# Optimization experiments

Hardware: AMD Instinct MI355X
Metric: run time of the kernel (lower is better)

The kernel has to match this reference:

```python
import jax, jax.numpy as jnp
import numpy as np

D_MODEL = 1024
NUM_HEADS = 16
D_K = D_MODEL // NUM_HEADS


def setup_inputs() -> dict:
    key = jax.random.key(0)
    ks = jax.random.split(key, 11)
    B, S = 2, 2048
    scale = 1.0 / np.sqrt(D_MODEL)
    inp = {
        "Q_in": jax.random.normal(ks[0], (B, S, D_MODEL), jnp.float32),
        "K_in": jax.random.normal(ks[1], (B, S, D_MODEL), jnp.float32),
        "V_in": jax.random.normal(ks[2], (B, S, D_MODEL), jnp.float32),
        "Wq": jax.random.normal(ks[3], (D_MODEL, D_MODEL), jnp.float32) * scale,
        "bq": jnp.zeros((D_MODEL,), jnp.float32),
        "Wk": jax.random.normal(ks[4], (D_MODEL, D_MODEL), jnp.float32) * scale,
        "bk": jnp.zeros((D_MODEL,), jnp.float32),
        "Wv": jax.random.normal(ks[5], (D_MODEL, D_MODEL), jnp.float32) * scale,
        "bv": jnp.zeros((D_MODEL,), jnp.float32),
        "Wfc": jax.random.normal(ks[6], (D_MODEL, D_MODEL), jnp.float32) * scale,
        "bfc": jnp.zeros((D_MODEL,), jnp.float32),
    }
    return inp


def _split_heads(x, B):
    # [B, S, D] -> [B, H, S, d_k]
    return x.reshape(B, -1, NUM_HEADS, D_K).transpose(0, 2, 1, 3)


def reference(Q_in, K_in, V_in, Wq, bq, Wk, bk, Wv, bv, Wfc, bfc):
    B = Q_in.shape[0]
    q = _split_heads(Q_in @ Wq + bq, B)
    k = _split_heads(K_in @ Wk + bk, B)
    v = _split_heads(V_in @ Wv + bv, B)
    # scaled dot-product attention (mask=None)
    scores = jnp.einsum("bhqd,bhkd->bhqk", q, k) / jnp.sqrt(jnp.float32(D_K))
    attn = jax.nn.softmax(scores, axis=-1)
    ctx = jnp.einsum("bhqk,bhkd->bhqd", attn, v)
    out = ctx.transpose(0, 2, 1, 3).reshape(B, -1, D_MODEL)
    out = out @ Wfc + bfc
    return out, attn
```

## Files before the change

### kernel.cpp

```cpp
#include <hip/hip_runtime.h>

typedef unsigned short u16;
typedef _Float16 f16;
typedef __attribute__((ext_vector_type(8))) f16 f16x8;
typedef __attribute__((ext_vector_type(4))) float f32x4;
typedef __attribute__((ext_vector_type(4))) u16 u16x4;
typedef __attribute__((ext_vector_type(8))) u16 u16x8;

__device__ __forceinline__ u16 f2h(float x){
  f16 h = (f16)x;
  return __builtin_bit_cast(u16, h);
}
__device__ __forceinline__ float h2f(u16 v){
  return (float)__builtin_bit_cast(f16, v);
}

__device__ __forceinline__ void stage16(const void* g, void* l){
  __builtin_amdgcn_global_load_lds(
      (const __attribute__((address_space(1))) unsigned*)g,
      (__attribute__((address_space(3))) unsigned*)l, 16, 0, 0);
}

__global__ __launch_bounds__(256) void convert_x3(
    const float* __restrict__ in0, const float* __restrict__ in1, const float* __restrict__ in2,
    u16* __restrict__ o0, u16* __restrict__ o1, u16* __restrict__ o2){
  const int b = blockIdx.x >> 12;
  const int i = (blockIdx.x & 4095) * 256 + threadIdx.x;
  const float* in = (b == 0) ? in0 : (b == 1) ? in1 : in2;
  u16* out = (b == 0) ? o0 : (b == 1) ? o1 : o2;
  f32x4 v = ((const f32x4*)in)[i];
  u16x4 h;
  #pragma unroll
  for (int j = 0; j < 4; j++) h[j] = f2h(v[j]);
  ((u16x4*)out)[i] = h;
}

__global__ __launch_bounds__(256) void transpose_w4(
    const float* __restrict__ W0, const float* __restrict__ W1,
    const float* __restrict__ W2, const float* __restrict__ W3,
    u16* __restrict__ t0, u16* __restrict__ t1, u16* __restrict__ t2, u16* __restrict__ t3){
  __shared__ float tile[64][68];
  const int z = blockIdx.z;
  const float* W = (z == 0) ? W0 : (z == 1) ? W1 : (z == 2) ? W2 : W3;
  u16* wt = (z == 0) ? t0 : (z == 1) ? t1 : (z == 2) ? t2 : t3;
  const int tid = threadIdx.x;
  const int k0 = blockIdx.y * 64, n0 = blockIdx.x * 64;
  #pragma unroll
  for (int g = 0; g < 4; g++){
    int flat4 = g * 256 + tid;
    int row = flat4 >> 4, c4 = flat4 & 15;
    f32x4 v = *(const f32x4*)&W[(size_t)(k0 + row) * 1024 + n0 + c4 * 4];
    *(f32x4*)&tile[row][c4 * 4] = v;
  }
  __syncthreads();
  const int n = tid >> 2, kc = (tid & 3) * 16;
  u16x8 o0, o1;
  #pragma unroll
  for (int j = 0; j < 8; j++){
    o0[j] = f2h(tile[kc + j][n]);
    o1[j] = f2h(tile[kc + 8 + j][n]);
  }
  u16* dst = &wt[(size_t)(n0 + n) * 1024 + k0 + kc];
  *(u16x8*)dst = o0;
  *(u16x8*)(dst + 8) = o1;
}

template<int MODE>
__device__ __forceinline__ void gemm_body(
    const u16* __restrict__ A, const u16* __restrict__ B,
    const float* __restrict__ bias,
    float* __restrict__ outF, u16* __restrict__ outH,
    int N, int K, int bx, int by)
{
  __shared__ u16 sA[128 * 32];
  __shared__ u16 sB[128 * 32];
  const int tid = threadIdx.x;
  const int wid = tid >> 6, lane = tid & 63;
  const int lm = lane & 15, lg = lane >> 4;
  const int bm = by * 128, bn = bx * 128;
  const int wrow = (wid >> 1) * 64, wcol = (wid & 1) * 64;
  const int srow = tid >> 2;
  const int skc  = (tid & 3) * 8;

  f32x4 acc[4][4] = {};

  for (int kt = 0; kt < K; kt += 32){
    {
      char* dA = (char*)sA + wid * 1024;
      char* dB = (char*)sB + wid * 1024;
      stage16(A + (size_t)(bm +      srow) * K + kt + skc, dA);
      stage16(A + (size_t)(bm + 64 + srow) * K + kt + skc, dA + 4096);
      stage16(B + (size_t)(bn +      srow) * K + kt + skc, dB);
      stage16(B + (size_t)(bn + 64 + srow) * K + kt + skc, dB + 4096);
    }
    __syncthreads();
    f16x8 af[4], bf[4];
    #pragma unroll
    for (int mf = 0; mf < 4; mf++)
      af[mf] = *(const f16x8*)&sA[(wrow + mf * 16 + lm) * 32 + lg * 8];
    #pragma unroll
    for (int nf = 0; nf < 4; nf++)
      bf[nf] = *(const f16x8*)&sB[(wcol + nf * 16 + lm) * 32 + lg * 8];
    #pragma unroll
    for (int mf = 0; mf < 4; mf++)
      #pragma unroll
      for (int nf = 0; nf < 4; nf++)
        acc[mf][nf] = __builtin_amdgcn_mfma_f32_16x16x32_f16(af[mf], bf[nf], acc[mf][nf], 0, 0, 0);
    __syncthreads();
  }

  #pragma unroll
  for (int mf = 0; mf < 4; mf++)
    #pragma unroll
    for (int nf = 0; nf < 4; nf++){
      const int n  = bn + wcol + nf * 16 + lm;
      const int mb = bm + wrow + mf * 16 + lg * 4;
      #pragma unroll
      for (int r = 0; r < 4; r++){
        const int m = mb + r;
        float v = acc[mf][nf][r] + ((MODE == 2) ? bias[m] : bias[n]);
        if constexpr (MODE == 0){
          outF[(size_t)m * N + n] = v;
        } else if constexpr (MODE == 1){
          const size_t idx = (((size_t)((m >> 11) * 16 + (n >> 6))) * 2048 + (m & 2047)) * 64 + (n & 63);
          outH[idx] = f2h(v);
        } else {
          const size_t idx = (((size_t)((n >> 11) * 16 + (m >> 6))) * 64 + (m & 63)) * 2048 + (n & 2047);
          outH[idx] = f2h(v);
        }
      }
    }
}

__global__ __launch_bounds__(256, 2) void gemm_qk(
    const u16* __restrict__ xq, const u16* __restrict__ wqt, const float* __restrict__ bq, u16* __restrict__ qh,
    const u16* __restrict__ xk, const u16* __restrict__ wkt, const float* __restrict__ bk, u16* __restrict__ kh){
  const int z = blockIdx.z;
  gemm_body<1>(z ? xk : xq, z ? wkt : wqt, z ? bk : bq, nullptr, z ? kh : qh,
               1024, 1024, blockIdx.x, blockIdx.y);
}

__global__ __launch_bounds__(256, 2) void gemm_v(
    const u16* __restrict__ wvt, const u16* __restrict__ xv, const float* __restrict__ bv, u16* __restrict__ vt){
  gemm_body<2>(wvt, xv, bv, nullptr, vt, 4096, 1024, blockIdx.x, blockIdx.y);
}

__global__ __launch_bounds__(256, 2) void gemm_fc(
    const u16* __restrict__ ctx, const u16* __restrict__ wft, const float* __restrict__ bfc, float* __restrict__ outF){
  gemm_body<0>(ctx, wft, bfc, outF, nullptr, 1024, 1024, blockIdx.x, blockIdx.y);
}

__global__ __launch_bounds__(256, 2) void attn_fused(
    const u16* __restrict__ qh_, const u16* __restrict__ kh_,
    const u16* __restrict__ vt_,
    float* __restrict__ attn_out, u16* __restrict__ ctx)
{
  constexpr int S = 2048;
  __shared__ __align__(16) char smem[4 * 16 * 520 * 2];
  __shared__ float sred[4][16];
  __shared__ float linv[16];
  const int tid = threadIdx.x, wid = tid >> 6, lane = tid & 63;
  const int lm = lane & 15, lg = lane >> 4;
  u16 (*pb)[520] = (u16 (*)[520])(smem + wid * (16 * 520 * 2));
  const int wg = blockIdx.x;
  const int xcd = wg & 7, li = wg >> 3;
  const int bh = (xcd << 2) + (li >> 7);
  const int q0 = (li & 127) * 16;
  const size_t base = (size_t)bh * S * 64;
  const u16* Qh = qh_ + base;
  const u16* Kh = kh_ + base;
  const u16* Vt = vt_ + base;
  float* Aout = attn_out + (size_t)bh * S * S;
  const int kbase = wid * 512;

  f16x8 qb[2];
  #pragma unroll
  for (int ks = 0; ks < 2; ks++)
    qb[ks] = *(const f16x8*)(Qh + (size_t)(q0 + lm) * 64 + ks * 32 + lg * 8);

  const float SCL2 = 0.18033688011112042f;

  float part = 0.0f;
  f32x4 cacc[4] = {};
  for (int nt2 = 0; nt2 < 16; nt2++){
    const int col0 = kbase + nt2 * 32;
    f16x8 vb[4];
    #pragma unroll
    for (int nf = 0; nf < 4; nf++)
      vb[nf] = *(const f16x8*)(Vt + (size_t)(nf * 16 + lm) * S + col0 + lg * 8);

    const u16* kp0 = Kh + (size_t)(col0 + lm) * 64 + lg * 8;
    const u16* kp1 = kp0 + 16 * 64;
    f16x8 k00 = *(const f16x8*)(kp0);
    f16x8 k01 = *(const f16x8*)(kp0 + 32);
    f16x8 k10 = *(const f16x8*)(kp1);
    f16x8 k11 = *(const f16x8*)(kp1 + 32);
    f32x4 c0 = {}, c1 = {};
    c0 = __builtin_amdgcn_mfma_f32_16x16x32_f16(k00, qb[0], c0, 0, 0, 0);
    c0 = __builtin_amdgcn_mfma_f32_16x16x32_f16(k01, qb[1], c0, 0, 0, 0);
    c1 = __builtin_amdgcn_mfma_f32_16x16x32_f16(k10, qb[0], c1, 0, 0, 0);
    c1 = __builtin_amdgcn_mfma_f32_16x16x32_f16(k11, qb[1], c1, 0, 0, 0);

    #pragma unroll
    for (int half = 0; half < 2; half++){
      f32x4 c = half ? c1 : c0;
      u16x4 hp;
      #pragma unroll
      for (int r = 0; r < 4; r++){
        float e = __builtin_amdgcn_exp2f(c[r] * SCL2);
        part += e;
        hp[r] = f2h(e);
      }
      *(u16x4*)&pb[lm][nt2 * 32 + half * 16 + lg * 4] = hp;
    }
    f16x8 pa = *(const f16x8*)&pb[lm][nt2 * 32 + lg * 8];
    #pragma unroll
    for (int nf = 0; nf < 4; nf++)
      cacc[nf] = __builtin_amdgcn_mfma_f32_16x16x32_f16(pa, vb[nf], cacc[nf], 0, 0, 0);
  }

  part += __shfl_xor(part, 16);
  part += __shfl_xor(part, 32);
  if (lane < 16) sred[wid][lm] = part;
  __syncthreads();
  if (tid < 16) linv[tid] = 1.0f / (sred[0][tid] + sred[1][tid] + sred[2][tid] + sred[3][tid]);
  __syncthreads();

  #pragma unroll 4
  for (int r = 0; r < 16; r++){
    u16x8 hv = *(const u16x8*)&pb[r][lane * 8];
    const float iv = linv[r];
    f32x4 lo = { h2f(hv[0]) * iv, h2f(hv[1]) * iv, h2f(hv[2]) * iv, h2f(hv[3]) * iv };
    f32x4 hi = { h2f(hv[4]) * iv, h2f(hv[5]) * iv, h2f(hv[6]) * iv, h2f(hv[7]) * iv };
    float* dst = Aout + (size_t)(q0 + r) * S + kbase + lane * 8;
    *(f32x4*)dst = lo;
    *(f32x4*)(dst + 4) = hi;
  }

  const float myinv = linv[lg * 4 + 0];
  (void)myinv;
  float iv4[4];
  #pragma unroll
  for (int r = 0; r < 4; r++) iv4[r] = linv[lg * 4 + r];

  __syncthreads();
  float (*cred)[64][20] = (float (*)[64][20])smem;
  #pragma unroll
  for (int nf = 0; nf < 4; nf++){
    f32x4 sc;
    #pragma unroll
    for (int r = 0; r < 4; r++) sc[r] = cacc[nf][r] * iv4[r];
    *(f32x4*)&cred[wid][nf * 16 + lm][lg * 4] = sc;
  }
  __syncthreads();
  const int b = bh >> 4, h = bh & 15;
  const int rd = lane;
  const int rq = wid * 4;
  f32x4 s0 = *(const f32x4*)&cred[0][rd][rq];
  f32x4 s1 = *(const f32x4*)&cred[1][rd][rq];
  f32x4 s2 = *(const f32x4*)&cred[2][rd][rq];
  f32x4 s3 = *(const f32x4*)&cred[3][rd][rq];
  #pragma unroll
  for (int j = 0; j < 4; j++){
    float v = s0[j] + s1[j] + s2[j] + s3[j];
    ctx[(size_t)(b * 2048 + q0 + rq + j) * 1024 + h * 64 + rd] = f2h(v);
  }
}

extern "C" void kernel_launch(void* const* d_in, const int* in_sizes, int n_in,
                              void* d_out, int out_size, void* d_ws, size_t ws_size,
                              hipStream_t stream) {
  const float* Qi  = (const float*)d_in[0];
  const float* Ki  = (const float*)d_in[1];
  const float* Vi  = (const float*)d_in[2];
  const float* Wq  = (const float*)d_in[3];
  const float* bq  = (const float*)d_in[4];
  const float* Wk  = (const float*)d_in[5];
  const float* bk  = (const float*)d_in[6];
  const float* Wv  = (const float*)d_in[7];
  const float* bv  = (const float*)d_in[8];
  const float* Wfc = (const float*)d_in[9];
  const float* bfc = (const float*)d_in[10];

  char* w = (char*)d_ws;
  const size_t P  = 8388608;
  const size_t PW = 2097152;
  u16* xq  = (u16*)(w + 0*P);
  u16* xk  = (u16*)(w + 1*P);
  u16* xv  = (u16*)(w + 2*P);
  u16* qh  = (u16*)(w + 3*P);
  u16* kh  = (u16*)(w + 4*P);
  u16* vt  = (u16*)(w + 5*P);
  u16* ctx = (u16*)(w + 6*P);
  char* w2 = w + 7*P;
  u16* wqt = (u16*)(w2 + 0*PW);
  u16* wkt = (u16*)(w2 + 1*PW);
  u16* wvt = (u16*)(w2 + 2*PW);
  u16* wft = (u16*)(w2 + 3*PW);

  float* outp  = (float*)d_out;
  float* attnp = outp + 4194304;

  convert_x3<<<12288, 256, 0, stream>>>(Qi, Ki, Vi, xq, xk, xv);
  transpose_w4<<<dim3(16, 16, 4), 256, 0, stream>>>(Wq, Wk, Wv, Wfc, wqt, wkt, wvt, wft);

  gemm_qk<<<dim3(8, 32, 2), 256, 0, stream>>>(xq, wqt, bq, qh, xk, wkt, bk, kh);
  gemm_v<<<dim3(32, 8), 256, 0, stream>>>(wvt, xv, bv, vt);
  attn_fused<<<4096, 256, 0, stream>>>(qh, kh, vt, attnp, ctx);
  gemm_fc<<<dim3(8, 32), 256, 0, stream>>>(ctx, wft, bfc, outp);
}
```

Measured before the change: 424.6 us.

## Merge V projection into QK GEMM launch and persist attention blocks with prefetch

The Q, K and V projection GEMMs now run as one launch, with blockIdx.z selecting the operand set and the V GEMM using swapped grid indices. The attention kernel drops from 4096 to 512 workgroups, and each workgroup loops over 8 query tiles. K/V fragments are prefetched two steps ahead in a triple-buffered register ring, and the attention row write-back uses narrower, more coalesced stores. The aim is to remove one kernel launch, cut per-block setup, and hide global load latency behind MFMA work, at the cost of higher register pressure and less parallelism in the attention grid.

```diff
diff --git a/kernel.cpp b/kernel.cpp
--- a/kernel.cpp
+++ b/kernel.cpp
@@ -132,23 +132,26 @@
     }
 }
 
-__global__ __launch_bounds__(256, 2) void gemm_qk(
+__global__ __launch_bounds__(256, 2) void gemm_qkv(
     const u16* __restrict__ xq, const u16* __restrict__ wqt, const float* __restrict__ bq, u16* __restrict__ qh,
-    const u16* __restrict__ xk, const u16* __restrict__ wkt, const float* __restrict__ bk, u16* __restrict__ kh){
+    const u16* __restrict__ xk, const u16* __restrict__ wkt, const float* __restrict__ bk, u16* __restrict__ kh,
+    const u16* __restrict__ wvt, const u16* __restrict__ xv, const float* __restrict__ bv, u16* __restrict__ vt){
   const int z = blockIdx.z;
-  gemm_body<1>(z ? xk : xq, z ? wkt : wqt, z ? bk : bq, nullptr, z ? kh : qh,
-               1024, 1024, blockIdx.x, blockIdx.y);
-}
-
-__global__ __launch_bounds__(256, 2) void gemm_v(
-    const u16* __restrict__ wvt, const u16* __restrict__ xv, const float* __restrict__ bv, u16* __restrict__ vt){
-  gemm_body<2>(wvt, xv, bv, nullptr, vt, 4096, 1024, blockIdx.x, blockIdx.y);
+  if (z == 2){
+    gemm_body<2>(wvt, xv, bv, nullptr, vt, 4096, 1024, blockIdx.y, blockIdx.x);
+  } else if (z == 1){
+    gemm_body<1>(xk, wkt, bk, nullptr, kh, 1024, 1024, blockIdx.x, blockIdx.y);
+  } else {
+    gemm_body<1>(xq, wqt, bq, nullptr, qh, 1024, 1024, blockIdx.x, blockIdx.y);
+  }
 }
 
 __global__ __launch_bounds__(256, 2) void gemm_fc(
     const u16* __restrict__ ctx, const u16* __restrict__ wft, const float* __restrict__ bfc, float* __restrict__ outF){
   gemm_body<0>(ctx, wft, bfc, outF, nullptr, 1024, 1024, blockIdx.x, blockIdx.y);
 }
+
+#define MFMA16(A, B, C) __builtin_amdgcn_mfma_f32_16x16x32_f16((A), (B), (C), 0, 0, 0)
 
 __global__ __launch_bounds__(256, 2) void attn_fused(
     const u16* __restrict__ qh_, const u16* __restrict__ kh_,
@@ -156,114 +159,131 @@
     float* __restrict__ attn_out, u16* __restrict__ ctx)
 {
   constexpr int S = 2048;
-  __shared__ __align__(16) char smem[4 * 16 * 520 * 2];
+  __shared__ __align__(16) char smem[4 * 16640];
   __shared__ float sred[4][16];
   __shared__ float linv[16];
   const int tid = threadIdx.x, wid = tid >> 6, lane = tid & 63;
   const int lm = lane & 15, lg = lane >> 4;
-  u16 (*pb)[520] = (u16 (*)[520])(smem + wid * (16 * 520 * 2));
-  const int wg = blockIdx.x;
-  const int xcd = wg & 7, li = wg >> 3;
-  const int bh = (xcd << 2) + (li >> 7);
-  const int q0 = (li & 127) * 16;
+  u16 (*pb)[520] = (u16 (*)[520])(smem + wid * 16640);
+  float (*credw)[20] = (float (*)[20])(smem + wid * 16640);
+
+  const int w = blockIdx.x;
+  const int l = w >> 3;
+  const int bh = (w & 7) * 4 + (l >> 4);
+  const int qtb = l & 15;
   const size_t base = (size_t)bh * S * 64;
   const u16* Qh = qh_ + base;
   const u16* Kh = kh_ + base;
   const u16* Vt = vt_ + base;
   float* Aout = attn_out + (size_t)bh * S * S;
   const int kbase = wid * 512;
-
-  f16x8 qb[2];
-  #pragma unroll
-  for (int ks = 0; ks < 2; ks++)
-    qb[ks] = *(const f16x8*)(Qh + (size_t)(q0 + lm) * 64 + ks * 32 + lg * 8);
-
+  const int b = bh >> 4, h = bh & 15;
   const float SCL2 = 0.18033688011112042f;
 
-  float part = 0.0f;
-  f32x4 cacc[4] = {};
-  for (int nt2 = 0; nt2 < 16; nt2++){
-    const int col0 = kbase + nt2 * 32;
-    f16x8 vb[4];
-    #pragma unroll
-    for (int nf = 0; nf < 4; nf++)
-      vb[nf] = *(const f16x8*)(Vt + (size_t)(nf * 16 + lm) * S + col0 + lg * 8);
-
-    const u16* kp0 = Kh + (size_t)(col0 + lm) * 64 + lg * 8;
-    const u16* kp1 = kp0 + 16 * 64;
-    f16x8 k00 = *(const f16x8*)(kp0);
-    f16x8 k01 = *(const f16x8*)(kp0 + 32);
-    f16x8 k10 = *(const f16x8*)(kp1);
-    f16x8 k11 = *(const f16x8*)(kp1 + 32);
-    f32x4 c0 = {}, c1 = {};
-    c0 = __builtin_amdgcn_mfma_f32_16x16x32_f16(k00, qb[0], c0, 0, 0, 0);
-    c0 = __builtin_amdgcn_mfma_f32_16x16x32_f16(k01, qb[1], c0, 0, 0, 0);
-    c1 = __builtin_amdgcn_mfma_f32_16x16x32_f16(k10, qb[0], c1, 0, 0, 0);
-    c1 = __builtin_amdgcn_mfma_f32_16x16x32_f16(k11, qb[1], c1, 0, 0, 0);
-
-    #pragma unroll
-    for (int half = 0; half < 2; half++){
-      f32x4 c = half ? c1 : c0;
-      u16x4 hp;
+  const u16* qrow = Qh + (size_t)lm * 64 + lg * 8;
+
+  for (int t = 0; t < 8; ++t){
+    const int q0 = (qtb + t * 16) * 16;
+    const u16* qp = qrow + (size_t)q0 * 64;
+    f16x8 qb0 = *(const f16x8*)(qp);
+    f16x8 qb1 = *(const f16x8*)(qp + 32);
+
+    f16x8 vs[3][4], ks4[3][4];
+    #define LOADF(nt2_, s_) do {                                              \
+      const int col0_ = kbase + (nt2_) * 32;                                  \
+      _Pragma("unroll")                                                       \
+      for (int nf_ = 0; nf_ < 4; nf_++)                                       \
+        vs[s_][nf_] = *(const f16x8*)(Vt + (size_t)(nf_ * 16 + lm) * S + col0_ + lg * 8); \
+      const u16* kp_ = Kh + (size_t)(col0_ + lm) * 64 + lg * 8;               \
+      ks4[s_][0] = *(const f16x8*)(kp_);                                      \
+      ks4[s_][1] = *(const f16x8*)(kp_ + 32);                                 \
+      ks4[s_][2] = *(const f16x8*)(kp_ + 1024);                               \
+      ks4[s_][3] = *(const f16x8*)(kp_ + 1024 + 32);                          \
+    } while (0)
+
+    LOADF(0, 0);
+    LOADF(1, 1);
+
+    float part = 0.0f;
+    f32x4 cacc[4] = {};
+    #pragma unroll
+    for (int nt2 = 0; nt2 < 16; ++nt2){
+      if (nt2 < 14) LOADF(nt2 + 2, (nt2 + 2) % 3);
+      const int cs = nt2 % 3;
+      f32x4 c0 = {}, c1 = {};
+      c0 = MFMA16(ks4[cs][0], qb0, c0);
+      c0 = MFMA16(ks4[cs][1], qb1, c0);
+      c1 = MFMA16(ks4[cs][2], qb0, c1);
+      c1 = MFMA16(ks4[cs][3], qb1, c1);
+      u16x4 hp0, hp1;
       #pragma unroll
       for (int r = 0; r < 4; r++){
-        float e = __builtin_amdgcn_exp2f(c[r] * SCL2);
-        part += e;
-        hp[r] = f2h(e);
-      }
-      *(u16x4*)&pb[lm][nt2 * 32 + half * 16 + lg * 4] = hp;
-    }
-    f16x8 pa = *(const f16x8*)&pb[lm][nt2 * 32 + lg * 8];
-    #pragma unroll
-    for (int nf = 0; nf < 4; nf++)
-      cacc[nf] = __builtin_amdgcn_mfma_f32_16x16x32_f16(pa, vb[nf], cacc[nf], 0, 0, 0);
-  }
-
-  part += __shfl_xor(part, 16);
-  part += __shfl_xor(part, 32);
-  if (lane < 16) sred[wid][lm] = part;
-  __syncthreads();
-  if (tid < 16) linv[tid] = 1.0f / (sred[0][tid] + sred[1][tid] + sred[2][tid] + sred[3][tid]);
-  __syncthreads();
-
-  #pragma unroll 4
-  for (int r = 0; r < 16; r++){
-    u16x8 hv = *(const u16x8*)&pb[r][lane * 8];
-    const float iv = linv[r];
-    f32x4 lo = { h2f(hv[0]) * iv, h2f(hv[1]) * iv, h2f(hv[2]) * iv, h2f(hv[3]) * iv };
-    f32x4 hi = { h2f(hv[4]) * iv, h2f(hv[5]) * iv, h2f(hv[6]) * iv, h2f(hv[7]) * iv };
-    float* dst = Aout + (size_t)(q0 + r) * S + kbase + lane * 8;
-    *(f32x4*)dst = lo;
-    *(f32x4*)(dst + 4) = hi;
-  }
-
-  const float myinv = linv[lg * 4 + 0];
-  (void)myinv;
-  float iv4[4];
-  #pragma unroll
-  for (int r = 0; r < 4; r++) iv4[r] = linv[lg * 4 + r];
-
-  __syncthreads();
-  float (*cred)[64][20] = (float (*)[64][20])smem;
-  #pragma unroll
-  for (int nf = 0; nf < 4; nf++){
-    f32x4 sc;
-    #pragma unroll
-    for (int r = 0; r < 4; r++) sc[r] = cacc[nf][r] * iv4[r];
-    *(f32x4*)&cred[wid][nf * 16 + lm][lg * 4] = sc;
-  }
-  __syncthreads();
-  const int b = bh >> 4, h = bh & 15;
-  const int rd = lane;
-  const int rq = wid * 4;
-  f32x4 s0 = *(const f32x4*)&cred[0][rd][rq];
-  f32x4 s1 = *(const f32x4*)&cred[1][rd][rq];
-  f32x4 s2 = *(const f32x4*)&cred[2][rd][rq];
-  f32x4 s3 = *(const f32x4*)&cred[3][rd][rq];
-  #pragma unroll
-  for (int j = 0; j < 4; j++){
-    float v = s0[j] + s1[j] + s2[j] + s3[j];
-    ctx[(size_t)(b * 2048 + q0 + rq + j) * 1024 + h * 64 + rd] = f2h(v);
+        float e = __builtin_amdgcn_exp2f(c0[r] * SCL2);
+        part += e; hp0[r] = f2h(e);
+      }
+      #pragma unroll
+      for (int r = 0; r < 4; r++){
+        float e = __builtin_amdgcn_exp2f(c1[r] * SCL2);
+        part += e; hp1[r] = f2h(e);
+      }
+      *(u16x4*)&pb[lm][nt2 * 32 + lg * 4] = hp0;
+      *(u16x4*)&pb[lm][nt2 * 32 + 16 + lg * 4] = hp1;
+      f16x8 pa = *(const f16x8*)&pb[lm][nt2 * 32 + lg * 8];
+      #pragma unroll
+      for (int nf = 0; nf < 4; nf++)
+        cacc[nf] = MFMA16(pa, vs[cs][nf], cacc[nf]);
+    }
+    #undef LOADF
+
+    part += __shfl_xor(part, 16);
+    part += __shfl_xor(part, 32);
+    if (lane < 16) sred[wid][lm] = part;
+    __syncthreads();
+    if (tid < 16) linv[tid] = 1.0f / (sred[0][tid] + sred[1][tid] + sred[2][tid] + sred[3][tid]);
+    __syncthreads();
+
+    #pragma unroll 2
+    for (int r = 0; r < 16; r++){
+      const float iv = linv[r];
+      float* rowp = Aout + (size_t)(q0 + r) * S + kbase;
+      #pragma unroll
+      for (int ch = 0; ch < 2; ch++){
+        u16x4 hv = *(const u16x4*)&pb[r][ch * 256 + lane * 4];
+        f32x4 av = { h2f(hv[0]) * iv, h2f(hv[1]) * iv, h2f(hv[2]) * iv, h2f(hv[3]) * iv };
+        *(f32x4*)(rowp + ch * 256 + lane * 4) = av;
+      }
+    }
+
+    __syncthreads();
+
+    float iv4[4];
+    #pragma unroll
+    for (int r = 0; r < 4; r++) iv4[r] = linv[lg * 4 + r];
+    #pragma unroll
+    for (int nf = 0; nf < 4; nf++){
+      f32x4 sc;
+      #pragma unroll
+      for (int r = 0; r < 4; r++) sc[r] = cacc[nf][r] * iv4[r];
+      *(f32x4*)&credw[nf * 16 + lm][lg * 4] = sc;
+    }
+    __syncthreads();
+    {
+      const float (*cr0)[20] = (const float (*)[20])(smem + 0 * 16640);
+      const float (*cr1)[20] = (const float (*)[20])(smem + 1 * 16640);
+      const float (*cr2)[20] = (const float (*)[20])(smem + 2 * 16640);
+      const float (*cr3)[20] = (const float (*)[20])(smem + 3 * 16640);
+      const int rd = lane, rq = wid * 4;
+      f32x4 s0 = *(const f32x4*)&cr0[rd][rq];
+      f32x4 s1 = *(const f32x4*)&cr1[rd][rq];
+      f32x4 s2 = *(const f32x4*)&cr2[rd][rq];
+      f32x4 s3 = *(const f32x4*)&cr3[rd][rq];
+      #pragma unroll
+      for (int j = 0; j < 4; j++){
+        float v = s0[j] + s1[j] + s2[j] + s3[j];
+        ctx[(size_t)(b * 2048 + q0 + rq + j) * 1024 + h * 64 + rd] = f2h(v);
+      }
+    }
+    __syncthreads();
   }
 }
 
@@ -304,8 +324,9 @@
   convert_x3<<<12288, 256, 0, stream>>>(Qi, Ki, Vi, xq, xk, xv);
   transpose_w4<<<dim3(16, 16, 4), 256, 0, stream>>>(Wq, Wk, Wv, Wfc, wqt, wkt, wvt, wft);
 
-  gemm_qk<<<dim3(8, 32, 2), 256, 0, stream>>>(xq, wqt, bq, qh, xk, wkt, bk, kh);
-  gemm_v<<<dim3(32, 8), 256, 0, stream>>>(wvt, xv, bv, vt);
-  attn_fused<<<4096, 256, 0, stream>>>(qh, kh, vt, attnp, ctx);
+  gemm_qkv<<<dim3(8, 32, 3), 256, 0, stream>>>(xq, wqt, bq, qh,
+                                               xk, wkt, bk, kh,
+                                               wvt, xv, bv, vt);
+  attn_fused<<<512, 256, 0, stream>>>(qh, kh, vt, attnp, ctx);
   gemm_fc<<<dim3(8, 32), 256, 0, stream>>>(ctx, wft, bfc, outp);
 }
```

Result: slower. 540.0 us (+27.2%).
